# Performance work log

Hardware: AMD Instinct MI355X
Metric: run time of the kernel (lower is better)

## Reference

```python
import jax, jax.numpy as jnp
import numpy as np

B, S, L = 2, 64, 256
H, C = 8, 64          # num_heads, dim_head
D = H * C             # embed_dim = 512
EPS = 1e-5


def layer_norm(x, gamma, beta):
    mu = jnp.mean(x, axis=-1, keepdims=True)
    var = jnp.mean(jnp.square(x - mu), axis=-1, keepdims=True)
    return (x - mu) * jax.lax.rsqrt(var + EPS) * gamma + beta


def setup_inputs() -> dict:
    key = jax.random.key(0)
    ks = jax.random.split(key, 9)
    s_in = 1.0 / np.sqrt(D)
    return {
        "x": jax.random.normal(ks[0], (B, S, L, D), dtype=jnp.float32),
        # nn.Linear(D, 3D): weight [3D, D], bias [3D]
        "w_row": jax.random.uniform(ks[1], (3 * D, D), jnp.float32, -s_in, s_in),
        "b_row": jax.random.uniform(ks[2], (3 * D,), jnp.float32, -s_in, s_in),
        "w_col": jax.random.uniform(ks[3], (3 * D, D), jnp.float32, -s_in, s_in),
        "b_col": jax.random.uniform(ks[4], (3 * D,), jnp.float32, -s_in, s_in),
        "g1": jnp.ones((D,), jnp.float32),
        "beta1": jnp.zeros((D,), jnp.float32),
        "g2": jnp.ones((D,), jnp.float32),
        "beta2": jnp.zeros((D,), jnp.float32),
    }


def reference(x, w_row, b_row, w_col, b_col, g1, beta1, g2, beta2):
    # ---- row attention (over L axis) ----
    qkv = jnp.einsum('bsld,ed->bsle', x, w_row) + b_row  # [B,S,L,3D]
    q, k, v = jnp.split(qkv, 3, axis=-1)
    q = q.reshape(B, S, L, H, C)
    k = k.reshape(B, S, L, H, C)
    v = v.reshape(B, S, L, H, C)
    # NOTE: original applies no 1/sqrt(dim_head) scaling
    row_attn = jnp.einsum('bsihc,bsjhc->bhsij', q, k)     # [B,H,S,L,L]
    row_attn = jax.nn.softmax(row_attn, axis=-1)
    row_out = jnp.einsum('bhsij,bsjhd->bsihd', row_attn, v).reshape(B, S, L, D)
    out = layer_norm(x + row_out, g1, beta1)

    # ---- column attention (over S axis) ----
    qkv = jnp.einsum('bsld,ed->bsle', out, w_col) + b_col
    q, k, v = jnp.split(qkv, 3, axis=-1)
    q = q.reshape(B, S, L, H, C)
    k = k.reshape(B, S, L, H, C)
    v = v.reshape(B, S, L, H, C)
    col_attn = jnp.einsum('bilhc,bjlhc->bhijl', q, k)     # [B,H,S,S,L]
    col_attn = jax.nn.softmax(col_attn, axis=-2)          # softmax over j (key rows)
    col_out = jnp.einsum('bhijl,bjlhd->bilhd', col_attn, v).reshape(B, S, L, D)
    out = layer_norm(out + col_out, g2, beta2)
    return out
```

## Files before the change

kernel.cpp:

```cpp
#include <hip/hip_runtime.h>

typedef unsigned short u16;
typedef unsigned int u32;
typedef float f32x4 __attribute__((ext_vector_type(4)));
typedef short s16x8 __attribute__((ext_vector_type(8)));

struct alignas(8) U16x4 { u16 a, b, c, d; };

#define DEV static __device__ __forceinline__

DEV u16 f2bf(float f) {
  u32 x = __float_as_uint(f);
  x += 0x7fffu + ((x >> 16) & 1u);
  return (u16)(x >> 16);
}
DEV float bf2f(u16 u) { return __uint_as_float(((u32)u) << 16); }
DEV f32x4 fz4() { f32x4 z = {0.f, 0.f, 0.f, 0.f}; return z; }

DEV void gl16(const u16* g, u16* l) {
  __builtin_amdgcn_global_load_lds(
      (const __attribute__((address_space(1))) u32*)g,
      (__attribute__((address_space(3))) u32*)l, 16, 0, 0);
}


__global__ __launch_bounds__(256) void k_cvt(const float* __restrict__ in,
                                             u16* __restrict__ outp, int n4) {
  int i = blockIdx.x * 256 + threadIdx.x;
  if (i < n4) {
    f32x4 v = reinterpret_cast<const f32x4*>(in)[i];
    U16x4 r = {f2bf(v.x), f2bf(v.y), f2bf(v.z), f2bf(v.w)};
    reinterpret_cast<U16x4*>(outp)[i] = r;
  }
}

template<int MODE>
__global__ __launch_bounds__(256) void k_gemm(
    const u16* __restrict__ A, const u16* __restrict__ W,
    const float* __restrict__ bias,
    u16* __restrict__ D0, u16* __restrict__ D1, u16* __restrict__ D2) {
  __shared__ u16 Sg[16384];
  const int lin = blockIdx.x;
  const int j = lin >> 3, xcd = lin & 7;
  const int bx = j % 12;
  const int by = xcd * 32 + j / 12;
  const int t = threadIdx.x;
  const int w = t >> 6, lane = t & 63, lr = lane & 15, lk = lane >> 4;
  const int wr = w >> 1, wc = w & 1;
  const bool vblk = (bx >= 8) && (MODE == 0);

  f32x4 acc[4][4];
#pragma unroll
  for (int i = 0; i < 4; i++)
#pragma unroll
    for (int jj = 0; jj < 4; jj++) acc[i][jj] = fz4();

  const int srow = w * 32 + (lane >> 2);
  const int scol = (lane & 3) * 8;
  const u16* Ap = A + (size_t)(by * 128 + srow) * 512 + scol;
  const u16* Wp = W + (size_t)(bx * 128 + srow) * 512 + scol;
  const int wb = w * 1024;

#define STAGE(kt_, buf_)                                            \
  {                                                                 \
    const int k_ = (kt_) * 32;                                      \
    gl16(Ap + k_, &Sg[(buf_) + wb]);                                \
    gl16(Ap + k_ + 16 * 512, &Sg[(buf_) + wb + 512]);               \
    gl16(Wp + k_, &Sg[(buf_) + 4096 + wb]);                         \
    gl16(Wp + k_ + 16 * 512, &Sg[(buf_) + 4096 + wb + 512]);        \
  }

#define COMPUTE(cur_)                                                             \
  {                                                                               \
    s16x8 aq[4], bq[4];                                                           \
    _Pragma("unroll")                                                             \
    for (int mi = 0; mi < 4; mi++)                                                \
      aq[mi] = *reinterpret_cast<const s16x8*>(                                   \
          &Sg[(cur_) + (wr * 64 + mi * 16 + lr) * 32 + lk * 8]);                  \
    _Pragma("unroll")                                                             \
    for (int ni = 0; ni < 4; ni++)                                                \
      bq[ni] = *reinterpret_cast<const s16x8*>(                                   \
          &Sg[(cur_) + 4096 + (wc * 64 + ni * 16 + lr) * 32 + lk * 8]);           \
    if (!vblk) {                                                                  \
      _Pragma("unroll")                                                           \
      for (int mi = 0; mi < 4; mi++)                                              \
        _Pragma("unroll")                                                         \
        for (int ni = 0; ni < 4; ni++)                                            \
          acc[mi][ni] = __builtin_amdgcn_mfma_f32_16x16x32_bf16(                  \
              aq[mi], bq[ni], acc[mi][ni], 0, 0, 0);                              \
    } else {                                                                      \
      _Pragma("unroll")                                                           \
      for (int mi = 0; mi < 4; mi++)                                              \
        _Pragma("unroll")                                                         \
        for (int ni = 0; ni < 4; ni++)                                            \
          acc[mi][ni] = __builtin_amdgcn_mfma_f32_16x16x32_bf16(                  \
              bq[ni], aq[mi], acc[mi][ni], 0, 0, 0);                              \
    }                                                                             \
  }

  STAGE(0, 0)

  for (int kt = 0; kt < 15; ++kt) {
    const int cur = (kt & 1) * 8192;
    const int nxt = 8192 - cur;
    STAGE(kt + 1, nxt)
    asm volatile("s_waitcnt vmcnt(4)" ::: "memory");
    asm volatile("s_barrier" ::: "memory");
    COMPUTE(cur)
    asm volatile("s_barrier" ::: "memory");
  }
  asm volatile("s_waitcnt vmcnt(0)" ::: "memory");
  asm volatile("s_barrier" ::: "memory");
  COMPUTE(8192)

#undef STAGE
#undef COMPUTE

  const int colg = bx * 2 + wc;
  if (MODE == 0) {
    const int bs = by >> 1;
    if (!vblk) {
      u16* dst = (colg < 8) ? D0 : D1;
      const int h = colg & 7;
      const size_t hb = (size_t)(bs * 8 + h) * 16384;
#pragma unroll
      for (int ni = 0; ni < 4; ni++) {
        const int c = ni * 16 + lr;
        const float bv = bias[(colg << 6) + c];
#pragma unroll
        for (int mi = 0; mi < 4; mi++) {
          const int l0 = (by & 1) * 128 + wr * 64 + mi * 16 + lk * 4;
#pragma unroll
          for (int q = 0; q < 4; q++)
            dst[hb + (size_t)(l0 + q) * 64 + c] = f2bf(acc[mi][ni][q] + bv);
        }
      }
    } else {
      const int h = colg & 7;
      const size_t hb = (size_t)(bs * 8 + h) * 16384;
#pragma unroll
      for (int ni = 0; ni < 4; ni++) {
        const int c0 = ni * 16 + lk * 4;
        const f32x4 bv4 = *reinterpret_cast<const f32x4*>(&bias[(colg << 6) + c0]);
#pragma unroll
        for (int mi = 0; mi < 4; mi++) {
          const int l = (by & 1) * 128 + wr * 64 + mi * 16 + lr;
#pragma unroll
          for (int q = 0; q < 4; q++)
            D2[hb + (size_t)(c0 + q) * 256 + l] = f2bf(acc[mi][ni][q] + bv4[q]);
        }
      }
    }
  } else {
    if (colg < 16) {
      u16* dst = (colg < 8) ? D0 : D1;
      const int h = colg & 7;
#pragma unroll
      for (int ni = 0; ni < 4; ni++) {
        const int c = ni * 16 + lr;
        const float bv = bias[(colg << 6) + c];
#pragma unroll
        for (int mi = 0; mi < 4; mi++) {
          const int r0 = by * 128 + wr * 64 + mi * 16 + lk * 4;
#pragma unroll
          for (int q = 0; q < 4; q++) {
            const int row = r0 + q;
            const int b = row >> 14, s = (row >> 8) & 63, l = row & 255;
            dst[(((size_t)(b * 256 + l) * 8 + h) * 64 + s) * 64 + c] = f2bf(acc[mi][ni][q] + bv);
          }
        }
      }
    } else {
#pragma unroll
      for (int ni = 0; ni < 4; ni++) {
        const int c512 = (bx - 8) * 128 + wc * 64 + ni * 16 + lr;
        const float bv = bias[1024 + c512];
#pragma unroll
        for (int mi = 0; mi < 4; mi++) {
          const int r0 = by * 128 + wr * 64 + mi * 16 + lk * 4;
#pragma unroll
          for (int q = 0; q < 4; q++)
            D2[(size_t)(r0 + q) * 512 + c512] = f2bf(acc[mi][ni][q] + bv);
        }
      }
    }
  }
}

__global__ __launch_bounds__(256) void k_row_attn(
    const u16* __restrict__ Qh, const u16* __restrict__ Kh,
    const u16* __restrict__ Vth, u16* __restrict__ O) {
  __shared__ u16 KP[256 * 72];
  __shared__ u16 Vt[64 * 264];
  const int lin = blockIdx.x;
  const int qt = (lin >> 3) & 3;
  const int bsh = (lin & 7) + (lin >> 5) * 8;
  const int h = bsh & 7, bs = bsh >> 3;
  const int t = threadIdx.x, w = t >> 6, lane = t & 63, lr = lane & 15, lk = lane >> 4;
  const u16* kg = Kh + (size_t)bsh * 16384;
  const u16* vg = Vth + (size_t)bsh * 16384;
#pragma unroll
  for (int u = 0; u < 8; u++)
    *reinterpret_cast<s16x8*>(&KP[t * 72 + u * 8]) =
        *reinterpret_cast<const s16x8*>(&kg[t * 64 + u * 8]);
#pragma unroll
  for (int i = 0; i < 8; i++) {
    const int id = i * 256 + t;
    const int r = id >> 5, ch = id & 31;
    *reinterpret_cast<s16x8*>(&Vt[r * 264 + ch * 8]) =
        *reinterpret_cast<const s16x8*>(&vg[r * 256 + ch * 8]);
  }
  const u16* qg = Qh + (size_t)bsh * 16384 + (size_t)(qt * 64 + w * 16 + lr) * 64 + lk * 8;
  const s16x8 aq0 = *reinterpret_cast<const s16x8*>(qg);
  const s16x8 aq1 = *reinterpret_cast<const s16x8*>(qg + 32);
  __syncthreads();

  f32x4 sc[16];
#pragma unroll
  for (int ni = 0; ni < 16; ni++) sc[ni] = fz4();
#pragma unroll
  for (int ni = 0; ni < 16; ni++) {
    const s16x8 b0 = *reinterpret_cast<const s16x8*>(&KP[(ni * 16 + lr) * 72 + lk * 8]);
    sc[ni] = __builtin_amdgcn_mfma_f32_16x16x32_bf16(aq0, b0, sc[ni], 0, 0, 0);
  }
#pragma unroll
  for (int ni = 0; ni < 16; ni++) {
    const s16x8 b1 = *reinterpret_cast<const s16x8*>(&KP[(ni * 16 + lr) * 72 + 32 + lk * 8]);
    sc[ni] = __builtin_amdgcn_mfma_f32_16x16x32_bf16(aq1, b1, sc[ni], 0, 0, 0);
  }
  float mx[4], sm[4];
#pragma unroll
  for (int qi = 0; qi < 4; qi++) {
    float m = sc[0][qi];
#pragma unroll
    for (int ni = 1; ni < 16; ni++) m = fmaxf(m, sc[ni][qi]);
    mx[qi] = m;
  }
#pragma unroll
  for (int d = 1; d < 16; d <<= 1)
#pragma unroll
    for (int qi = 0; qi < 4; qi++) mx[qi] = fmaxf(mx[qi], __shfl_xor(mx[qi], d));
#pragma unroll
  for (int qi = 0; qi < 4; qi++) sm[qi] = 0.f;
#pragma unroll
  for (int ni = 0; ni < 16; ni++)
#pragma unroll
    for (int qi = 0; qi < 4; qi++) {
      const float p = __expf(sc[ni][qi] - mx[qi]);
      sc[ni][qi] = p;
      sm[qi] += p;
    }
#pragma unroll
  for (int d = 1; d < 16; d <<= 1)
#pragma unroll
    for (int qi = 0; qi < 4; qi++) sm[qi] += __shfl_xor(sm[qi], d);
  float inv[4];
#pragma unroll
  for (int qi = 0; qi < 4; qi++) inv[qi] = 1.f / sm[qi];
  __syncthreads();
#pragma unroll
  for (int ni = 0; ni < 16; ni++)
#pragma unroll
    for (int qi = 0; qi < 4; qi++)
      KP[(w * 16 + lk * 4 + qi) * 264 + ni * 16 + lr] = f2bf(sc[ni][qi] * inv[qi]);
  __syncthreads();

  f32x4 o[4];
#pragma unroll
  for (int mi = 0; mi < 4; mi++) o[mi] = fz4();
#pragma unroll
  for (int ks = 0; ks < 8; ks++) {
    const s16x8 vb = *reinterpret_cast<const s16x8*>(&Vt[(w * 16 + lr) * 264 + ks * 32 + lk * 8]);
#pragma unroll
    for (int mi = 0; mi < 4; mi++) {
      const s16x8 pa = *reinterpret_cast<const s16x8*>(&KP[(mi * 16 + lr) * 264 + ks * 32 + lk * 8]);
      o[mi] = __builtin_amdgcn_mfma_f32_16x16x32_bf16(pa, vb, o[mi], 0, 0, 0);
    }
  }
  const size_t ob = (size_t)bs * 131072 + (size_t)qt * 64 * 512 + h * 64 + w * 16 + lr;
#pragma unroll
  for (int mi = 0; mi < 4; mi++)
#pragma unroll
    for (int qi = 0; qi < 4; qi++)
      O[ob + (size_t)(mi * 16 + lk * 4 + qi) * 512] = f2bf(o[mi][qi]);
}

__global__ __launch_bounds__(256) void k_col(
    const u16* __restrict__ Qc, const u16* __restrict__ Kc,
    const u16* __restrict__ V2, u16* __restrict__ O) {
  __shared__ u16 Qs[64][72];
  __shared__ u16 Ks[64][72];
  __shared__ u16 Pl[64][72];
  __shared__ u16 Vt[64][72];
  __shared__ float red[2][64][2];
  const int bid = blockIdx.x;
  const int h = bid & 7, bl = bid >> 3;
  const int l_ = bl & 255, b = bl >> 8;
  const size_t base = ((size_t)(b * 256 + l_) * 8 + h) * 4096;
  const int t = threadIdx.x;
  const int r = t >> 2, c0 = (t & 3) * 16;
  *reinterpret_cast<s16x8*>(&Qs[r][c0]) = *reinterpret_cast<const s16x8*>(&Qc[base + r * 64 + c0]);
  *reinterpret_cast<s16x8*>(&Qs[r][c0 + 8]) = *reinterpret_cast<const s16x8*>(&Qc[base + r * 64 + c0 + 8]);
  *reinterpret_cast<s16x8*>(&Ks[r][c0]) = *reinterpret_cast<const s16x8*>(&Kc[base + r * 64 + c0]);
  *reinterpret_cast<s16x8*>(&Ks[r][c0 + 8]) = *reinterpret_cast<const s16x8*>(&Kc[base + r * 64 + c0 + 8]);
  __syncthreads();
  const int w = t >> 6, l = t & 63, lr = l & 15, lk = l >> 4;
  const int wr = w >> 1, wc = w & 1;
  f32x4 acc[2][2];
#pragma unroll
  for (int i = 0; i < 2; i++)
#pragma unroll
    for (int jj = 0; jj < 2; jj++) acc[i][jj] = fz4();
#pragma unroll
  for (int ks = 0; ks < 2; ks++) {
    s16x8 aq[2], bq[2];
#pragma unroll
    for (int mi = 0; mi < 2; mi++)
      aq[mi] = *reinterpret_cast<const s16x8*>(&Qs[wr * 32 + mi * 16 + lr][ks * 32 + lk * 8]);
#pragma unroll
    for (int ni = 0; ni < 2; ni++)
      bq[ni] = *reinterpret_cast<const s16x8*>(&Ks[wc * 32 + ni * 16 + lr][ks * 32 + lk * 8]);
#pragma unroll
    for (int mi = 0; mi < 2; mi++)
#pragma unroll
      for (int ni = 0; ni < 2; ni++)
        acc[mi][ni] = __builtin_amdgcn_mfma_f32_16x16x32_bf16(aq[mi], bq[ni], acc[mi][ni], 0, 0, 0);
  }
  float mloc[2][4];
#pragma unroll
  for (int mi = 0; mi < 2; mi++)
#pragma unroll
    for (int q = 0; q < 4; q++) mloc[mi][q] = fmaxf(acc[mi][0][q], acc[mi][1][q]);
#pragma unroll
  for (int d = 1; d < 16; d <<= 1)
#pragma unroll
    for (int mi = 0; mi < 2; mi++)
#pragma unroll
      for (int q = 0; q < 4; q++)
        mloc[mi][q] = fmaxf(mloc[mi][q], __shfl_xor(mloc[mi][q], d));
  if (lr == 0)
#pragma unroll
    for (int mi = 0; mi < 2; mi++)
#pragma unroll
      for (int q = 0; q < 4; q++) red[0][wr * 32 + mi * 16 + lk * 4 + q][wc] = mloc[mi][q];
  __syncthreads();
  float mg[2][4], ss[2][4];
#pragma unroll
  for (int mi = 0; mi < 2; mi++)
#pragma unroll
    for (int q = 0; q < 4; q++) {
      const int r0 = wr * 32 + mi * 16 + lk * 4 + q;
      mg[mi][q] = fmaxf(red[0][r0][0], red[0][r0][1]);
      ss[mi][q] = 0.f;
    }
#pragma unroll
  for (int mi = 0; mi < 2; mi++)
#pragma unroll
    for (int ni = 0; ni < 2; ni++)
#pragma unroll
      for (int q = 0; q < 4; q++) {
        const float p = __expf(acc[mi][ni][q] - mg[mi][q]);
        acc[mi][ni][q] = p;
        ss[mi][q] += p;
      }
#pragma unroll
  for (int d = 1; d < 16; d <<= 1)
#pragma unroll
    for (int mi = 0; mi < 2; mi++)
#pragma unroll
      for (int q = 0; q < 4; q++) ss[mi][q] += __shfl_xor(ss[mi][q], d);
  if (lr == 0)
#pragma unroll
    for (int mi = 0; mi < 2; mi++)
#pragma unroll
      for (int q = 0; q < 4; q++) red[1][wr * 32 + mi * 16 + lk * 4 + q][wc] = ss[mi][q];
  __syncthreads();
#pragma unroll
  for (int mi = 0; mi < 2; mi++)
#pragma unroll
    for (int q = 0; q < 4; q++) {
      const int r0 = wr * 32 + mi * 16 + lk * 4 + q;
      const float inv = 1.f / (red[1][r0][0] + red[1][r0][1]);
#pragma unroll
      for (int ni = 0; ni < 2; ni++)
        Pl[r0][wc * 32 + ni * 16 + lr] = f2bf(acc[mi][ni][q] * inv);
    }
  __syncthreads();
  {
    const u16* vg = V2 + ((size_t)(b * 64) * 256 + l_) * 512 + h * 64;
#pragma unroll
    for (int u = 0; u < 4; u++) {
      U16x4 vv = *reinterpret_cast<const U16x4*>(&vg[(size_t)r * 131072 + c0 + u * 4]);
      Vt[c0 + u * 4 + 0][r] = vv.a; Vt[c0 + u * 4 + 1][r] = vv.b;
      Vt[c0 + u * 4 + 2][r] = vv.c; Vt[c0 + u * 4 + 3][r] = vv.d;
    }
  }
  __syncthreads();
  f32x4 acc2[2][2];
#pragma unroll
  for (int i = 0; i < 2; i++)
#pragma unroll
    for (int jj = 0; jj < 2; jj++) acc2[i][jj] = fz4();
#pragma unroll
  for (int ks = 0; ks < 2; ks++) {
    s16x8 ap[2], bp[2];
#pragma unroll
    for (int mi = 0; mi < 2; mi++)
      ap[mi] = *reinterpret_cast<const s16x8*>(&Pl[wr * 32 + mi * 16 + lr][ks * 32 + lk * 8]);
#pragma unroll
    for (int ni = 0; ni < 2; ni++)
      bp[ni] = *reinterpret_cast<const s16x8*>(&Vt[wc * 32 + ni * 16 + lr][ks * 32 + lk * 8]);
#pragma unroll
    for (int mi = 0; mi < 2; mi++)
#pragma unroll
      for (int ni = 0; ni < 2; ni++)
        acc2[mi][ni] = __builtin_amdgcn_mfma_f32_16x16x32_bf16(ap[mi], bp[ni], acc2[mi][ni], 0, 0, 0);
  }
  const size_t ob = ((size_t)b * 16384 + l_) * 512 + h * 64;
#pragma unroll
  for (int mi = 0; mi < 2; mi++)
#pragma unroll
    for (int ni = 0; ni < 2; ni++)
#pragma unroll
      for (int q = 0; q < 4; q++) {
        const int i = wr * 32 + mi * 16 + lk * 4 + q;
        const int cc = wc * 32 + ni * 16 + lr;
        O[ob + (size_t)i * 131072 + cc] = f2bf(acc2[mi][ni][q]);
      }
}

__global__ __launch_bounds__(256) void k_ln1(
    const float* __restrict__ xin, const u16* __restrict__ add,
    const float* __restrict__ g, const float* __restrict__ be,
    u16* __restrict__ outp) {
  const int w = threadIdx.x >> 6, l = threadIdx.x & 63;
  const size_t row = (size_t)blockIdx.x * 4 + w;
  const size_t o = row * 512 + l * 8;
  f32x4 x0 = *reinterpret_cast<const f32x4*>(xin + o);
  f32x4 x1 = *reinterpret_cast<const f32x4*>(xin + o + 4);
  U16x4 a0 = *reinterpret_cast<const U16x4*>(add + o);
  U16x4 a1 = *reinterpret_cast<const U16x4*>(add + o + 4);
  float v[8] = {x0.x + bf2f(a0.a), x0.y + bf2f(a0.b), x0.z + bf2f(a0.c), x0.w + bf2f(a0.d),
                x1.x + bf2f(a1.a), x1.y + bf2f(a1.b), x1.z + bf2f(a1.c), x1.w + bf2f(a1.d)};
  float s = 0.f, sq = 0.f;
#pragma unroll
  for (int i = 0; i < 8; i++) { s += v[i]; sq += v[i] * v[i]; }
#pragma unroll
  for (int d = 1; d < 64; d <<= 1) { s += __shfl_xor(s, d); sq += __shfl_xor(sq, d); }
  const float mu = s * (1.f / 512.f);
  const float var = sq * (1.f / 512.f) - mu * mu;
  const float rstd = rsqrtf(fmaxf(var, 0.f) + 1e-5f);
  U16x4 r0, r1;
  const float* gp = g + l * 8;
  const float* bp = be + l * 8;
  r0.a = f2bf((v[0] - mu) * rstd * gp[0] + bp[0]);
  r0.b = f2bf((v[1] - mu) * rstd * gp[1] + bp[1]);
  r0.c = f2bf((v[2] - mu) * rstd * gp[2] + bp[2]);
  r0.d = f2bf((v[3] - mu) * rstd * gp[3] + bp[3]);
  r1.a = f2bf((v[4] - mu) * rstd * gp[4] + bp[4]);
  r1.b = f2bf((v[5] - mu) * rstd * gp[5] + bp[5]);
  r1.c = f2bf((v[6] - mu) * rstd * gp[6] + bp[6]);
  r1.d = f2bf((v[7] - mu) * rstd * gp[7] + bp[7]);
  *reinterpret_cast<U16x4*>(outp + o) = r0;
  *reinterpret_cast<U16x4*>(outp + o + 4) = r1;
}

__global__ __launch_bounds__(256) void k_ln2(
    const u16* __restrict__ xin, const u16* __restrict__ add,
    const float* __restrict__ g, const float* __restrict__ be,
    float* __restrict__ outp) {
  const int w = threadIdx.x >> 6, l = threadIdx.x & 63;
  const size_t row = (size_t)blockIdx.x * 4 + w;
  const size_t o = row * 512 + l * 8;
  U16x4 x0 = *reinterpret_cast<const U16x4*>(xin + o);
  U16x4 x1 = *reinterpret_cast<const U16x4*>(xin + o + 4);
  U16x4 a0 = *reinterpret_cast<const U16x4*>(add + o);
  U16x4 a1 = *reinterpret_cast<const U16x4*>(add + o + 4);
  float v[8] = {bf2f(x0.a) + bf2f(a0.a), bf2f(x0.b) + bf2f(a0.b),
                bf2f(x0.c) + bf2f(a0.c), bf2f(x0.d) + bf2f(a0.d),
                bf2f(x1.a) + bf2f(a1.a), bf2f(x1.b) + bf2f(a1.b),
                bf2f(x1.c) + bf2f(a1.c), bf2f(x1.d) + bf2f(a1.d)};
  float s = 0.f, sq = 0.f;
#pragma unroll
  for (int i = 0; i < 8; i++) { s += v[i]; sq += v[i] * v[i]; }
#pragma unroll
  for (int d = 1; d < 64; d <<= 1) { s += __shfl_xor(s, d); sq += __shfl_xor(sq, d); }
  const float mu = s * (1.f / 512.f);
  const float var = sq * (1.f / 512.f) - mu * mu;
  const float rstd = rsqrtf(fmaxf(var, 0.f) + 1e-5f);
  f32x4 g0 = *reinterpret_cast<const f32x4*>(g + l * 8);
  f32x4 g1v = *reinterpret_cast<const f32x4*>(g + l * 8 + 4);
  f32x4 b0 = *reinterpret_cast<const f32x4*>(be + l * 8);
  f32x4 b1 = *reinterpret_cast<const f32x4*>(be + l * 8 + 4);
  f32x4 o0, o1;
  o0.x = (v[0] - mu) * rstd * g0.x + b0.x;
  o0.y = (v[1] - mu) * rstd * g0.y + b0.y;
  o0.z = (v[2] - mu) * rstd * g0.z + b0.z;
  o0.w = (v[3] - mu) * rstd * g0.w + b0.w;
  o1.x = (v[4] - mu) * rstd * g1v.x + b1.x;
  o1.y = (v[5] - mu) * rstd * g1v.y + b1.y;
  o1.z = (v[6] - mu) * rstd * g1v.z + b1.z;
  o1.w = (v[7] - mu) * rstd * g1v.w + b1.w;
  *reinterpret_cast<f32x4*>(outp + o) = o0;
  *reinterpret_cast<f32x4*>(outp + o + 4) = o1;
}

extern "C" void kernel_launch(void* const* d_in, const int* in_sizes, int n_in,
                              void* d_out, int out_size, void* d_ws, size_t ws_size,
                              hipStream_t stream) {
  const float* x     = (const float*)d_in[0];
  const float* w_row = (const float*)d_in[1];
  const float* b_row = (const float*)d_in[2];
  const float* w_col = (const float*)d_in[3];
  const float* b_col = (const float*)d_in[4];
  const float* g1    = (const float*)d_in[5];
  const float* be1   = (const float*)d_in[6];
  const float* g2    = (const float*)d_in[7];
  const float* be2   = (const float*)d_in[8];
  float* out = (float*)d_out;
  char* ws = (char*)d_ws;

  u16* abf   = (u16*)(ws);
  u16* Qh    = (u16*)(ws + 33554432);
  u16* Kh    = (u16*)(ws + 67108864);
  u16* Vth   = (u16*)(ws + 100663296);
  u16* attnb = (u16*)(ws + 134217728);
  u16* out1b = (u16*)(ws + 167772160);
  u16* wbf   = (u16*)(ws + 201326592);
  const size_t NEED = 202899456;
  if (ws_size < NEED) {
    hipMemsetAsync(d_out, 0, (size_t)out_size * 4, stream);
    return;
  }
  u16* Qc2 = abf;
  u16* Kc2 = Qh;
  u16* V2  = Kh;

  k_cvt<<<16384, 256, 0, stream>>>(x, abf, 4194304);
  k_cvt<<<768, 256, 0, stream>>>(w_row, wbf, 196608);
  k_gemm<0><<<3072, 256, 0, stream>>>(abf, wbf, b_row, Qh, Kh, Vth);
  k_row_attn<<<4096, 256, 0, stream>>>(Qh, Kh, Vth, attnb);
  k_ln1<<<8192, 256, 0, stream>>>(x, attnb, g1, be1, out1b);

  k_cvt<<<768, 256, 0, stream>>>(w_col, wbf, 196608);
  k_gemm<1><<<3072, 256, 0, stream>>>(out1b, wbf, b_col, Qc2, Kc2, V2);
  k_col<<<4096, 256, 0, stream>>>(Qc2, Kc2, V2, attnb);
  k_ln2<<<8192, 256, 0, stream>>>(out1b, attnb, g2, be2, out);
}
```

Baseline: 411.5 us.

## Triple-buffer GEMM LDS pipeline and feed bf16 residual into first layernorm

The projection GEMM moves from double to triple buffering of its LDS tiles. It keeps two K-tiles of global-to-LDS loads in flight, waiting on vmcnt(8) instead of vmcnt(4), so memory latency is better hidden behind the MFMA work. Separately, the first layernorm now reads the bf16 copy of x already produced for the GEMM instead of the fp32 input, which halves that residual read. The costs are 50% more LDS per block, which may lower occupancy, and a residual that is now rounded to bf16.

```diff
diff --git a/kernel.cpp b/kernel.cpp
--- a/kernel.cpp
+++ b/kernel.cpp
@@ -39,7 +39,7 @@
     const u16* __restrict__ A, const u16* __restrict__ W,
     const float* __restrict__ bias,
     u16* __restrict__ D0, u16* __restrict__ D1, u16* __restrict__ D2) {
-  __shared__ u16 Sg[16384];
+  __shared__ u16 Sg[24576];
   const int lin = blockIdx.x;
   const int j = lin >> 3, xcd = lin & 7;
   const int bx = j % 12;
@@ -64,23 +64,25 @@
 #define STAGE(kt_, buf_)                                            \
   {                                                                 \
     const int k_ = (kt_) * 32;                                      \
-    gl16(Ap + k_, &Sg[(buf_) + wb]);                                \
-    gl16(Ap + k_ + 16 * 512, &Sg[(buf_) + wb + 512]);               \
-    gl16(Wp + k_, &Sg[(buf_) + 4096 + wb]);                         \
-    gl16(Wp + k_ + 16 * 512, &Sg[(buf_) + 4096 + wb + 512]);        \
+    const int b_ = (buf_) * 8192;                                   \
+    gl16(Ap + k_, &Sg[b_ + wb]);                                    \
+    gl16(Ap + k_ + 16 * 512, &Sg[b_ + wb + 512]);                   \
+    gl16(Wp + k_, &Sg[b_ + 4096 + wb]);                             \
+    gl16(Wp + k_ + 16 * 512, &Sg[b_ + 4096 + wb + 512]);            \
   }
 
 #define COMPUTE(cur_)                                                             \
   {                                                                               \
+    const int c_ = (cur_) * 8192;                                                 \
     s16x8 aq[4], bq[4];                                                           \
     _Pragma("unroll")                                                             \
     for (int mi = 0; mi < 4; mi++)                                                \
       aq[mi] = *reinterpret_cast<const s16x8*>(                                   \
-          &Sg[(cur_) + (wr * 64 + mi * 16 + lr) * 32 + lk * 8]);                  \
+          &Sg[c_ + (wr * 64 + mi * 16 + lr) * 32 + lk * 8]);                      \
     _Pragma("unroll")                                                             \
     for (int ni = 0; ni < 4; ni++)                                                \
       bq[ni] = *reinterpret_cast<const s16x8*>(                                   \
-          &Sg[(cur_) + 4096 + (wc * 64 + ni * 16 + lr) * 32 + lk * 8]);           \
+          &Sg[c_ + 4096 + (wc * 64 + ni * 16 + lr) * 32 + lk * 8]);               \
     if (!vblk) {                                                                  \
       _Pragma("unroll")                                                           \
       for (int mi = 0; mi < 4; mi++)                                              \
@@ -99,19 +101,22 @@
   }
 
   STAGE(0, 0)
-
-  for (int kt = 0; kt < 15; ++kt) {
-    const int cur = (kt & 1) * 8192;
-    const int nxt = 8192 - cur;
-    STAGE(kt + 1, nxt)
-    asm volatile("s_waitcnt vmcnt(4)" ::: "memory");
+  STAGE(1, 1)
+
+  for (int kt = 0; kt < 14; ++kt) {
+    STAGE(kt + 2, (kt + 2) % 3)
+    asm volatile("s_waitcnt vmcnt(8)" ::: "memory");
     asm volatile("s_barrier" ::: "memory");
-    COMPUTE(cur)
+    COMPUTE(kt % 3)
     asm volatile("s_barrier" ::: "memory");
   }
+  asm volatile("s_waitcnt vmcnt(4)" ::: "memory");
+  asm volatile("s_barrier" ::: "memory");
+  COMPUTE(2)
+  asm volatile("s_barrier" ::: "memory");
   asm volatile("s_waitcnt vmcnt(0)" ::: "memory");
   asm volatile("s_barrier" ::: "memory");
-  COMPUTE(8192)
+  COMPUTE(0)
 
 #undef STAGE
 #undef COMPUTE
@@ -430,18 +435,20 @@
 }
 
 __global__ __launch_bounds__(256) void k_ln1(
-    const float* __restrict__ xin, const u16* __restrict__ add,
+    const u16* __restrict__ xin, const u16* __restrict__ add,
     const float* __restrict__ g, const float* __restrict__ be,
     u16* __restrict__ outp) {
   const int w = threadIdx.x >> 6, l = threadIdx.x & 63;
   const size_t row = (size_t)blockIdx.x * 4 + w;
   const size_t o = row * 512 + l * 8;
-  f32x4 x0 = *reinterpret_cast<const f32x4*>(xin + o);
-  f32x4 x1 = *reinterpret_cast<const f32x4*>(xin + o + 4);
+  U16x4 x0 = *reinterpret_cast<const U16x4*>(xin + o);
+  U16x4 x1 = *reinterpret_cast<const U16x4*>(xin + o + 4);
   U16x4 a0 = *reinterpret_cast<const U16x4*>(add + o);
   U16x4 a1 = *reinterpret_cast<const U16x4*>(add + o + 4);
-  float v[8] = {x0.x + bf2f(a0.a), x0.y + bf2f(a0.b), x0.z + bf2f(a0.c), x0.w + bf2f(a0.d),
-                x1.x + bf2f(a1.a), x1.y + bf2f(a1.b), x1.z + bf2f(a1.c), x1.w + bf2f(a1.d)};
+  float v[8] = {bf2f(x0.a) + bf2f(a0.a), bf2f(x0.b) + bf2f(a0.b),
+                bf2f(x0.c) + bf2f(a0.c), bf2f(x0.d) + bf2f(a0.d),
+                bf2f(x1.a) + bf2f(a1.a), bf2f(x1.b) + bf2f(a1.b),
+                bf2f(x1.c) + bf2f(a1.c), bf2f(x1.d) + bf2f(a1.d)};
   float s = 0.f, sq = 0.f;
 #pragma unroll
   for (int i = 0; i < 8; i++) { s += v[i]; sq += v[i] * v[i]; }
@@ -540,7 +547,7 @@
   k_cvt<<<768, 256, 0, stream>>>(w_row, wbf, 196608);
   k_gemm<0><<<3072, 256, 0, stream>>>(abf, wbf, b_row, Qh, Kh, Vth);
   k_row_attn<<<4096, 256, 0, stream>>>(Qh, Kh, Vth, attnb);
-  k_ln1<<<8192, 256, 0, stream>>>(x, attnb, g1, be1, out1b);
+  k_ln1<<<8192, 256, 0, stream>>>(abf, attnb, g1, be1, out1b);
 
   k_cvt<<<768, 256, 0, stream>>>(w_col, wbf, 196608);
   k_gemm<1><<<3072, 256, 0, stream>>>(out1b, wbf, b_col, Qc2, Kc2, V2);
```

After: 380.0 us. 7.6% less time.
